# Kernel optimization log

Measured on AMD Instinct MI355X. Metric: run time of the kernel, lower is better.

Reference implementation:

```python
import jax, jax.numpy as jnp
import numpy as np

M1, M2, M3 = 12, 12, 8
WIDTH = 32


def _spectral_conv(v, wr, wi):
    # v: [B, C, X, Y, T]; wr/wi: [4, Ci, Co, M1, M2, M3]
    B, C, X, Y, T = v.shape
    vft = jnp.fft.rfftn(v, axes=(-3, -2, -1))  # [B,C,X,Y,T//2+1] complex
    w = wr.astype(jnp.complex64) + 1j * wi.astype(jnp.complex64)
    mul = lambda blk, ww: jnp.einsum('bixyz,ioxyz->boxyz', blk, ww)
    out = jnp.zeros((B, wr.shape[2], X, Y, T // 2 + 1), dtype=vft.dtype)
    out = out.at[:, :, :M1, :M2, :M3].set(mul(vft[:, :, :M1, :M2, :M3], w[0]))
    out = out.at[:, :, -M1:, :M2, :M3].set(mul(vft[:, :, -M1:, :M2, :M3], w[1]))
    out = out.at[:, :, :M1, -M2:, :M3].set(mul(vft[:, :, :M1, -M2:, :M3], w[2]))
    out = out.at[:, :, -M1:, -M2:, :M3].set(mul(vft[:, :, -M1:, -M2:, :M3], w[3]))
    return jnp.fft.irfftn(out, s=(X, Y, T), axes=(-3, -2, -1))


def _conv1x1(v, w, b):
    # v: [B,C,X,Y,T]; w: [Co,Ci]; b: [Co]
    return jnp.einsum('bixyz,oi->boxyz', v, w) + b[None, :, None, None, None]


def setup_inputs() -> dict:
    key = jax.random.key(0)
    ks = jax.random.split(key, 24)
    B, X, Y, T = 8, 64, 64, 40
    W = WIDTH
    scale = 1.0 / (W * W)
    d = {}
    d['h'] = jax.random.normal(ks[0], (B, X, Y, T, 2), dtype=jnp.float32)
    d['x'] = jax.random.normal(ks[1], (B, X, Y, T, 3), dtype=jnp.float32)
    d['fc0_w'] = jax.random.normal(ks[2], (5, W), dtype=jnp.float32) * 0.3
    d['fc0_b'] = jnp.zeros((W,), dtype=jnp.float32)
    for i, name in enumerate(['sc0', 'sc1', 'sc3']):
        d[name + '_wr'] = scale * jax.random.uniform(ks[3 + 2 * i], (4, W, W, M1, M2, M3), dtype=jnp.float32)
        d[name + '_wi'] = scale * jax.random.uniform(ks[4 + 2 * i], (4, W, W, M1, M2, M3), dtype=jnp.float32)
    for i, name in enumerate(['w0', 'w1', 'w3']):
        d[name + '_w'] = jax.random.normal(ks[9 + 2 * i], (W, W), dtype=jnp.float32) * (1.0 / np.sqrt(W))
        d[name + '_b'] = jnp.zeros((W,), dtype=jnp.float32)
    d['fc1_w'] = jax.random.normal(ks[15], (W, 64), dtype=jnp.float32) * (1.0 / np.sqrt(W))
    d['fc1_b'] = jnp.zeros((64,), dtype=jnp.float32)
    d['fc2_w'] = jax.random.normal(ks[16], (64, 2), dtype=jnp.float32) * 0.125
    d['fc2_b'] = jnp.zeros((2,), dtype=jnp.float32)
    return d


def reference(h, x, fc0_w, fc0_b, sc0_wr, sc0_wi, sc1_wr, sc1_wi, sc3_wr, sc3_wi,
              w0_w, w0_b, w1_w, w1_b, w3_w, w3_b, fc1_w, fc1_b, fc2_w, fc2_b):
    v = jnp.concatenate((h, x), axis=-1)                 # [B,X,Y,T,5]
    v = v @ fc0_w + fc0_b                                # lift to width
    v = jnp.transpose(v, (0, 4, 1, 2, 3))                # [B,W,X,Y,T]
    v = jax.nn.gelu(_spectral_conv(v, sc0_wr, sc0_wi) + _conv1x1(v, w0_w, w0_b), approximate=False)
    v = jax.nn.gelu(_spectral_conv(v, sc1_wr, sc1_wi) + _conv1x1(v, w1_w, w1_b), approximate=False)
    v = _spectral_conv(v, sc3_wr, sc3_wi) + _conv1x1(v, w3_w, w3_b)
    v = jnp.transpose(v, (0, 2, 3, 4, 1))                # [B,X,Y,T,W]
    v = jax.nn.gelu(v @ fc1_w + fc1_b, approximate=False)
    return v @ fc2_w + fc2_b                             # [B,X,Y,T,2]
```

## Files before the change

kernel.cpp:

```cpp
#include <hip/hip_runtime.h>
#include <math.h>

#define BATCH 8
#define WID   32
#define NX    64
#define NY    64
#define NT    40
#define M1C   12
#define KT    8
#define KXC   24
#define KYC   24
#define NXY   (NX*NY)
#define NXYT  (NXY*NT)
#define NP    (BATCH*NXYT)

#define TWO_PI 6.283185307179586f

static __device__ __forceinline__ float gelu_f(float v){
  return 0.5f*v*(1.0f + erff(v*0.7071067811865476f));
}

static __device__ __forceinline__ void barrier_lds(){
  asm volatile("s_waitcnt lgkmcnt(0)\n\ts_barrier" ::: "memory");
}


template<bool LIFT>
__global__ __launch_bounds__(512) void k_fwd_ty(const float* __restrict__ V, float2* __restrict__ F2,
                                                const float* __restrict__ hin, const float* __restrict__ xin,
                                                const float* __restrict__ lw, const float* __restrict__ lb){
  __shared__ __align__(16) unsigned char smem[56320];
  float2* twy   = (float2*)(smem+43008);
  float2* f2out = (float2*)smem;
  float*  wT2   = (float*)(smem+55296);
  int tid = threadIdx.x;
  int h = tid >> 8, t8 = tid & 255;
  int b = blockIdx.x >> 6, x = blockIdx.x & 63;
  int c = t8 & 31, k = t8 >> 5;
  if constexpr(LIFT){
    if(tid<192){
      int c4=tid/24, rem=tid-24*c4, i=rem>>2, e=rem&3;
      wT2[tid] = (i<5)? lw[i*32 + 4*c4 + e] : 2.0f*lb[4*c4+e];
    }
    __syncthreads();
  }
  for(int i=tid;i<KYC*NY;i+=512){
    int ky=i>>6, y=i&63;
    int f = ky<M1C ? ky : ky+40;
    float ang = -TWO_PI*(float)((f*y)%NY)/(float)NY;
    twy[i] = make_float2(cosf(ang), sinf(ang));
  }
  float2 twr[20];
  #pragma unroll
  for(int t=0;t<20;t++){
    float ang = -TWO_PI*(float)((k*t)%NT)/(float)NT;
    twr[t] = make_float2(cosf(ang), sinf(ang));
  }
  int toff = (k&1)*20;
  float2 acc[KYC];
  #pragma unroll
  for(int q=0;q<KYC;q++) acc[q]=make_float2(0.f,0.f);
  const float4* src = (const float4*)(V + (size_t)(b*NX+x)*(NY*NT*WID));
  const float* hb = hin + (size_t)(b*NX+x)*(NY*NT)*2;
  const float* xb = xin + (size_t)(b*NX+x)*(NY*NT)*3;
  float* myb0 = (float*)(smem + h*21504);
  float* myb1 = myb0 + 2688;

  int s0 = t8;
  int c40 = s0&7, t0s = (s0>>3)%20, yl0 = s0/160;
  bool has1 = (t8 < 64);
  int s1 = t8 + 256;
  int c41 = s1&7, t1s = (s1>>3)%20, yl1 = s1/160;

  float4 pa0, pb0, pa1, pb1;
  float2 hA0,hB0,hA1,hB1;
  float xA00,xA01,xA02,xB00,xB01,xB02;
  float xA10,xA11,xA12,xB10,xB11,xB12;

#define TY_LOAD(G) do{ \
    if constexpr(LIFT){ \
      { size_t pt = (size_t)((2*(G)+yl0)*40 + t0s); \
        hA0 = *(const float2*)(hb + pt*2); \
        hB0 = *(const float2*)(hb + (pt+20)*2); \
        xA00 = xb[pt*3]; xA01 = xb[pt*3+1]; xA02 = xb[pt*3+2]; \
        xB00 = xb[(pt+20)*3]; xB01 = xb[(pt+20)*3+1]; xB02 = xb[(pt+20)*3+2]; } \
      if(has1){ size_t pt = (size_t)((2*(G)+yl1)*40 + t1s); \
        hA1 = *(const float2*)(hb + pt*2); \
        hB1 = *(const float2*)(hb + (pt+20)*2); \
        xA10 = xb[pt*3]; xA11 = xb[pt*3+1]; xA12 = xb[pt*3+2]; \
        xB10 = xb[(pt+20)*3]; xB11 = xb[(pt+20)*3+1]; xB12 = xb[(pt+20)*3+2]; } \
    } else { \
      pa0 = src[(2*(G) + yl0)*320 + t0s*8 + c40]; \
      pb0 = src[(2*(G) + yl0)*320 + t0s*8 + c40 + 160]; \
      if(has1){ \
        pa1 = src[(2*(G) + yl1)*320 + t1s*8 + c41]; \
        pb1 = src[(2*(G) + yl1)*320 + t1s*8 + c41 + 160]; \
      } \
    } \
  }while(0)

#define TY_STAGE(BUF) do{ \
    if constexpr(LIFT){ \
      const float* wrp = wT2 + c40*24; \
      float4 w0v = *(const float4*)(wrp); \
      float4 w1v = *(const float4*)(wrp+4); \
      float4 w2v = *(const float4*)(wrp+8); \
      float4 w3v = *(const float4*)(wrp+12); \
      float4 w4v = *(const float4*)(wrp+16); \
      float4 wbv = *(const float4*)(wrp+20); \
      float su0=hA0.x+hB0.x, su1=hA0.y+hB0.y, su2=xA00+xB00, su3=xA01+xB01, su4=xA02+xB02; \
      float sd0=hA0.x-hB0.x, sd1=hA0.y-hB0.y, sd2=xA00-xB00, sd3=xA01-xB01, sd4=xA02-xB02; \
      float* bse = (BUF) + yl0*1344 + t0s; \
      _Pragma("unroll") \
      for(int e=0;e<4;e++){ \
        float w0=((float*)&w0v)[e], w1=((float*)&w1v)[e], w2=((float*)&w2v)[e]; \
        float w3=((float*)&w3v)[e], w4=((float*)&w4v)[e], wb=((float*)&wbv)[e]; \
        bse[(4*c40+e)*42]      = wb + su0*w0 + su1*w1 + su2*w2 + su3*w3 + su4*w4; \
        bse[(4*c40+e)*42 + 20] =      sd0*w0 + sd1*w1 + sd2*w2 + sd3*w3 + sd4*w4; \
      } \
      if(has1){ \
        float tu0=hA1.x+hB1.x, tu1=hA1.y+hB1.y, tu2=xA10+xB10, tu3=xA11+xB11, tu4=xA12+xB12; \
        float td0=hA1.x-hB1.x, td1=hA1.y-hB1.y, td2=xA10-xB10, td3=xA11-xB11, td4=xA12-xB12; \
        float* bs1 = (BUF) + yl1*1344 + t1s; \
        _Pragma("unroll") \
        for(int e=0;e<4;e++){ \
          float w0=((float*)&w0v)[e], w1=((float*)&w1v)[e], w2=((float*)&w2v)[e]; \
          float w3=((float*)&w3v)[e], w4=((float*)&w4v)[e], wb=((float*)&wbv)[e]; \
          bs1[(4*c41+e)*42]      = wb + tu0*w0 + tu1*w1 + tu2*w2 + tu3*w3 + tu4*w4; \
          bs1[(4*c41+e)*42 + 20] =      td0*w0 + td1*w1 + td2*w2 + td3*w3 + td4*w4; \
        } \
      } \
    } else { \
      float* bse = (BUF) + yl0*1344 + t0s; \
      _Pragma("unroll") \
      for(int e=0;e<4;e++){ \
        float av=((float*)&pa0)[e], bv=((float*)&pb0)[e]; \
        bse[(4*c40+e)*42]      = av+bv; \
        bse[(4*c40+e)*42 + 20] = av-bv; \
      } \
      if(has1){ \
        float* bs1 = (BUF) + yl1*1344 + t1s; \
        _Pragma("unroll") \
        for(int e=0;e<4;e++){ \
          float av=((float*)&pa1)[e], bv=((float*)&pb1)[e]; \
          bs1[(4*c41+e)*42]      = av+bv; \
          bs1[(4*c41+e)*42 + 20] = av-bv; \
        } \
      } \
    } \
  }while(0)

  TY_LOAD(h);
  TY_STAGE(myb0);
  TY_LOAD(h+2);
  __syncthreads();

  #pragma unroll 1
  for(int it=0; it<16; ++it){
    int g = 2*it + h;
    const float* vb = (it&1) ? myb1 : myb0;
    float*       vn = (it&1) ? myb0 : myb1;
    if(it+1<16){
      TY_STAGE(vn);
      if(it+2<16){
        TY_LOAD(g+4);
      }
    }
    {
      const float* vp0 = vb + c*42 + toff;
      const float* vp1 = vp0 + 1344;
      float sr0=0.f,si0=0.f,sr1=0.f,si1=0.f;
      #pragma unroll
      for(int i5=0; i5<5; i5++){
        float2 a0 = *(const float2*)(vp0 + i5*4);
        float2 b0 = *(const float2*)(vp0 + i5*4 + 2);
        float2 a1 = *(const float2*)(vp1 + i5*4);
        float2 b1 = *(const float2*)(vp1 + i5*4 + 2);
        float2 w0=twr[i5*4], w1=twr[i5*4+1], w2=twr[i5*4+2], w3=twr[i5*4+3];
        sr0 += a0.x*w0.x + a0.y*w1.x + b0.x*w2.x + b0.y*w3.x;
        si0 += a0.x*w0.y + a0.y*w1.y + b0.x*w2.y + b0.y*w3.y;
        sr1 += a1.x*w0.x + a1.y*w1.x + b1.x*w2.x + b1.y*w3.x;
        si1 += a1.x*w0.y + a1.y*w1.y + b1.x*w2.y + b1.y*w3.y;
      }
      int y = 2*g;
      #pragma unroll
      for(int q=0;q<KYC;q++){
        float4 wy = *(const float4*)&twy[q*NY + y];
        acc[q].x += sr0*wy.x - si0*wy.y + sr1*wy.z - si1*wy.w;
        acc[q].y += sr0*wy.y + si0*wy.x + sr1*wy.w + si1*wy.z;
      }
    }
    barrier_lds();
  }
  if(h==0){
    #pragma unroll
    for(int q=0;q<KYC;q++) f2out[c*193 + q*8 + k] = acc[q];
  }
  __syncthreads();
  if(h==1){
    #pragma unroll
    for(int q=0;q<KYC;q++){
      float2 v = f2out[c*193 + q*8 + k];
      f2out[c*193 + q*8 + k] = make_float2(v.x+acc[q].x, v.y+acc[q].y);
    }
  }
  __syncthreads();
  for(int i=tid;i<WID*KYC*KT;i+=512){
    int cc=i/192, e=i-cc*192;
    F2[((size_t)(b*WID+cc)*NX + x)*(KYC*KT) + e] = f2out[cc*193 + e];
  }
#undef TY_LOAD
#undef TY_STAGE
}

__global__ __launch_bounds__(256) void k_fwd_x(const float2* __restrict__ F2, float2* __restrict__ F3){
  __shared__ float2 tile[NX*KT];
  __shared__ float2 twi[KXC*65];
  int tid=threadIdx.x;
  int bc = blockIdx.x / KYC;
  int ky = blockIdx.x - bc*KYC;
  for(int i=tid;i<NX*KT;i+=256){
    int xx=i/KT, kt=i-xx*KT;
    tile[i] = F2[((size_t)bc*NX + xx)*(KYC*KT) + ky*KT + kt];
  }
  for(int i=tid;i<KXC*NX;i+=256){
    int kx=i/NX, xx=i-kx*NX;
    int f = kx<M1C ? kx : kx+40;
    float ang = -TWO_PI*(float)((f*xx)%NX)/(float)NX;
    twi[kx*65+xx] = make_float2(cosf(ang), sinf(ang));
  }
  __syncthreads();
  for(int item=tid; item<KXC*KT; item+=256){
    int kx=item/KT, kt=item-kx*KT;
    float sr=0.f, si=0.f;
    #pragma unroll 8
    for(int xx=0;xx<NX;xx++){
      float2 a = tile[xx*KT+kt];
      float2 w = twi[kx*65+xx];
      sr += a.x*w.x - a.y*w.y;
      si += a.x*w.y + a.y*w.x;
    }
    F3[(size_t)bc*(KXC*KYC*KT) + kx*(KYC*KT) + ky*KT + kt] = make_float2(sr,si);
  }
}

__global__ __launch_bounds__(256) void k_mix(const float2* __restrict__ F3, const float* __restrict__ wr,
                                             const float* __restrict__ wi, float2* __restrict__ F4){
  __shared__ float2 f3s[BATCH*WID*KT];
  int tid = threadIdx.x;
  int kx = blockIdx.x / KYC, ky = blockIdx.x - kx*KYC;
  int mode0 = blockIdx.x * KT;
  int xp = (kx>=M1C), yp = (ky>=M1C);
  int m1 = kx - M1C*xp, m2 = ky - M1C*yp;
  int blk = xp + 2*yp;
  for(int i=tid;i<1024;i+=256){
    int row=i>>2, q=i&3;
    ((float4*)f3s)[row*4+q] = ((const float4*)(F3 + (size_t)row*4608 + mode0))[q];
  }
  int o = tid>>3, kt = tid&7;
  size_t wbase = (size_t)blk*1179648 + (size_t)o*1152 + m1*96 + m2*8 + kt;
  float wre[WID], wim[WID];
  #pragma unroll
  for(int i=0;i<WID;i++){
    wre[i] = wr[wbase + (size_t)i*36864];
    wim[i] = wi[wbase + (size_t)i*36864];
  }
  __syncthreads();
  #pragma unroll
  for(int b=0;b<BATCH;b++){
    float ar=0.f, ai=0.f;
    #pragma unroll
    for(int i=0;i<WID;i++){
      float2 a = f3s[(b*WID+i)*KT + kt];
      ar += a.x*wre[i] - a.y*wim[i];
      ai += a.x*wim[i] + a.y*wre[i];
    }
    F4[(size_t)(b*WID+o)*4608 + mode0 + kt] = make_float2(ar,ai);
  }
}

__global__ __launch_bounds__(256) void k_inv_x(const float2* __restrict__ F4, float2* __restrict__ F2){
  __shared__ float2 tile[KXC*KT];
  __shared__ float2 twi[NX*25];
  int tid=threadIdx.x;
  int bc = blockIdx.x / KYC, ky = blockIdx.x - (blockIdx.x/KYC)*KYC;
  for(int i=tid;i<KXC*KT;i+=256){
    int kx=i/KT, kt=i-kx*KT;
    tile[i] = F4[(size_t)bc*4608 + kx*(KYC*KT) + ky*KT + kt];
  }
  for(int i=tid;i<NX*KXC;i+=256){
    int xx=i/KXC, kx=i-xx*KXC;
    int f = kx<M1C ? kx : kx+40;
    float ang = TWO_PI*(float)((f*xx)%NX)/(float)NX;
    twi[xx*25+kx] = make_float2(cosf(ang)*(1.0f/64.0f), sinf(ang)*(1.0f/64.0f));
  }
  __syncthreads();
  for(int item=tid; item<NX*KT; item+=256){
    int xx=item/KT, kt=item-xx*KT;
    float sr=0.f, si=0.f;
    #pragma unroll 8
    for(int kx=0;kx<KXC;kx++){
      float2 a = tile[kx*KT+kt];
      float2 w = twi[xx*25+kx];
      sr += a.x*w.x - a.y*w.y;
      si += a.x*w.y + a.y*w.x;
    }
    F2[((size_t)bc*NX + xx)*(KYC*KT) + ky*KT + kt] = make_float2(sr,si);
  }
}

template<bool GELU, bool LIFT>
__global__ __launch_bounds__(256) void k_conv(const float2* __restrict__ F2, const float* __restrict__ wcv,
                                              const float* __restrict__ bcv, float* __restrict__ V,
                                              const float* __restrict__ hin, const float* __restrict__ xin,
                                              const float* __restrict__ lw, const float* __restrict__ lb){
  __shared__ __align__(16) unsigned char smem[35840];
  float*  vtA  = (float*)smem;
  float*  vtB  = (float*)(smem+10240);
  float2* ftc0 = (float2*)(smem+20480);
  float2* ftc1 = (float2*)(smem+24576);
  float2* twy  = (float2*)(smem+28672);
  float*  wT2  = (float*)(smem+34816);
  float2* f2h  = (float2*)smem;

  int tid=threadIdx.x;
  int b  = blockIdx.x >> 7;
  int x  = (blockIdx.x >> 1) & 63;
  int y0 = (blockIdx.x & 1) * 32;
  int cid = tid & 31, ktid = tid >> 5;
  int oid = tid & 31, tg  = tid >> 5;

  if constexpr(LIFT){
    if(tid<192){
      int c4=tid/24, rem=tid-24*c4, i=rem>>2, e=rem&3;
      wT2[tid] = (i<5)? lw[i*32 + 4*c4 + e] : lb[4*c4+e];
    }
  }

  float2 fr[KYC];
  #pragma unroll
  for(int half=0; half<2; half++){
    for(int i=tid;i<1536;i+=256){
      int cc=i/96, q=i-cc*96;
      ((float4*)f2h)[i] = *((const float4*)(F2 + ((size_t)(b*WID + half*16 + cc)*NX + x)*(KYC*KT)) + q);
    }
    __syncthreads();
    if((cid>>4) == half){
      const float2* fp = f2h + (cid&15)*192 + ktid;
      #pragma unroll
      for(int ky=0;ky<KYC;ky++) fr[ky] = fp[ky*8];
    }
    __syncthreads();
  }
  {
    float ts = (ktid==0 ? 1.0f : 2.0f) * (1.0f/(float)NT);
    #pragma unroll
    for(int ky=0;ky<KYC;ky++){ fr[ky].x *= ts; fr[ky].y *= ts; }
  }
  float wreg[WID];
  #pragma unroll
  for(int cc=0;cc<WID;cc++) wreg[cc] = wcv[oid*WID + cc];
  float breg = bcv[oid];
  float2 twtg[KT];
  #pragma unroll
  for(int k=0;k<KT;k++){
    float ang = 0.78539816339744831f*(float)((k*tg)&7);
    twtg[k] = make_float2(cosf(ang), sinf(ang));
  }
  for(int i=tid;i<32*KYC;i+=256){
    int yy=i/KYC, ky=i-yy*KYC;
    int f = ky<M1C ? ky : ky+40;
    float ang = TWO_PI*(float)((f*(y0+yy))%NY)/(float)NY;
    twy[i] = make_float2(cosf(ang)*(1.0f/64.0f), sinf(ang)*(1.0f/64.0f));
  }
  float* plane = V + (size_t)((b*NX+x)*NY + y0)*(NT*WID);
  const float4* gp = (const float4*)plane;
  const float* hbc = hin + (size_t)((b*NX+x)*NY + y0)*NT*2;
  const float* xbc = xin + (size_t)((b*NX+x)*NY + y0)*NT*3;
  bool has3 = tid < 128;
  int t0c = tid>>3;
  int yy1c = (tid>=64);
  int t1c = yy1c ? ((tid-64)>>3) : ((tid+256)>>3);
  int t2c = (tid+192)>>3;
  int c4c = tid&7;

  float4 rA, rB, rC;
  float2 hC0, hC1, hC2;
  float xC00,xC01,xC02,xC10,xC11,xC12,xC20,xC21,xC22;

#define CV_LOAD(P) do{ \
    if constexpr(LIFT){ \
      { size_t pt = (size_t)((2*(P))*40 + t0c); \
        hC0 = *(const float2*)(hbc + pt*2); \
        xC00 = xbc[pt*3]; xC01 = xbc[pt*3+1]; xC02 = xbc[pt*3+2]; } \
      { size_t pt = (size_t)((2*(P)+yy1c)*40 + t1c); \
        hC1 = *(const float2*)(hbc + pt*2); \
        xC10 = xbc[pt*3]; xC11 = xbc[pt*3+1]; xC12 = xbc[pt*3+2]; } \
      if(has3){ size_t pt = (size_t)((2*(P)+1)*40 + t2c); \
        hC2 = *(const float2*)(hbc + pt*2); \
        xC20 = xbc[pt*3]; xC21 = xbc[pt*3+1]; xC22 = xbc[pt*3+2]; } \
    } else { \
      const float4* q = gp + (size_t)(P)*640; \
      rA = q[tid]; rB = q[256+tid]; \
      if(has3) rC = q[512+tid]; \
    } \
  }while(0)

#define CV_STAGE(BUF) do{ \
    if constexpr(LIFT){ \
      const float* wrp = wT2 + c4c*24; \
      float4 w0v = *(const float4*)(wrp); \
      float4 w1v = *(const float4*)(wrp+4); \
      float4 w2v = *(const float4*)(wrp+8); \
      float4 w3v = *(const float4*)(wrp+12); \
      float4 w4v = *(const float4*)(wrp+16); \
      float4 wbv = *(const float4*)(wrp+20); \
      float4 v0, v1, v2; \
      _Pragma("unroll") \
      for(int e=0;e<4;e++){ \
        float w0=((float*)&w0v)[e], w1=((float*)&w1v)[e], w2=((float*)&w2v)[e]; \
        float w3=((float*)&w3v)[e], w4=((float*)&w4v)[e], wb=((float*)&wbv)[e]; \
        ((float*)&v0)[e] = wb + hC0.x*w0 + hC0.y*w1 + xC00*w2 + xC01*w3 + xC02*w4; \
        ((float*)&v1)[e] = wb + hC1.x*w0 + hC1.y*w1 + xC10*w2 + xC11*w3 + xC12*w4; \
        if(has3) ((float*)&v2)[e] = wb + hC2.x*w0 + hC2.y*w1 + xC20*w2 + xC21*w3 + xC22*w4; \
      } \
      ((float4*)(BUF))[tid] = v0; \
      ((float4*)(BUF))[256+tid] = v1; \
      if(has3) ((float4*)(BUF))[512+tid] = v2; \
    } else { \
      ((float4*)(BUF))[tid] = rA; \
      ((float4*)(BUF))[256+tid] = rB; \
      if(has3) ((float4*)(BUF))[512+tid] = rC; \
    } \
  }while(0)

  CV_LOAD(0);
  CV_STAGE(vtA);
  CV_LOAD(1);
  __syncthreads();

  constexpr float CJ[KT][5] = {
    {1.f, 1.f,          1.f,          1.f,          1.f         },
    {1.f, 0.98768834f,  0.95105652f,  0.89100652f,  0.80901699f },
    {1.f, 0.95105652f,  0.80901699f,  0.58778525f,  0.30901699f },
    {1.f, 0.89100652f,  0.58778525f,  0.15643447f, -0.30901699f },
    {1.f, 0.80901699f,  0.30901699f, -0.30901699f, -0.80901699f },
    {1.f, 0.70710678f,  0.f,         -0.70710678f, -1.f         },
    {1.f, 0.58778525f, -0.30901699f, -0.95105652f, -0.80901699f },
    {1.f, 0.45399050f, -0.58778525f, -0.98768834f, -0.30901699f },
  };
  constexpr float SJ[KT][5] = {
    {0.f, 0.f,          0.f,          0.f,          0.f         },
    {0.f, 0.15643447f,  0.30901699f,  0.45399050f,  0.58778525f },
    {0.f, 0.30901699f,  0.58778525f,  0.80901699f,  0.95105652f },
    {0.f, 0.45399050f,  0.80901699f,  0.98768834f,  0.95105652f },
    {0.f, 0.58778525f,  0.95105652f,  0.95105652f,  0.58778525f },
    {0.f, 0.70710678f,  1.f,          0.70710678f,  0.f         },
    {0.f, 0.80901699f,  0.95105652f,  0.30901699f, -0.58778525f },
    {0.f, 0.89100652f,  0.80901699f, -0.15643447f, -0.95105652f },
  };

  #pragma unroll 1
  for(int it=0; it<16; ++it){
    float*  vcur = (it&1) ? vtB  : vtA;
    float*  vnxt = (it&1) ? vtA  : vtB;
    float2* fcur = (it&1) ? ftc1 : ftc0;
    int yl = it*2;
    {
      const float2* tw0 = twy + (size_t)yl*KYC;
      const float2* tw1 = tw0 + KYC;
      float sr0=0.f, si0=0.f, sr1=0.f, si1=0.f;
      #pragma unroll
      for(int ky=0;ky<KYC;ky+=2){
        float2 a  = fr[ky];
        float2 b2 = fr[ky+1];
        float4 w0 = *(const float4*)&tw0[ky];
        float4 w1 = *(const float4*)&tw1[ky];
        sr0 += a.x*w0.x - a.y*w0.y + b2.x*w0.z - b2.y*w0.w;
        si0 += a.x*w0.y + a.y*w0.x + b2.x*w0.w + b2.y*w0.z;
        sr1 += a.x*w1.x - a.y*w1.y + b2.x*w1.z - b2.y*w1.w;
        si1 += a.x*w1.y + a.y*w1.x + b2.x*w1.w + b2.y*w1.z;
      }
      fcur[      ktid*32 + cid] = make_float2(sr0,si0);
      fcur[256 + ktid*32 + cid] = make_float2(sr1,si1);
    }
    barrier_lds();
    if(it+1 < 16){
      CV_STAGE(vnxt);
    }
    if(it+2 < 16){
      CV_LOAD(it+2);
    }
    #pragma unroll
    for(int yy=0; yy<2; yy++){
      const float2* fsrc = fcur + yy*256;
      const float*  vb   = vcur + yy*1280;
      float* outp = plane + (size_t)(yl+yy)*(NT*WID);
      float acc[5];
      #pragma unroll
      for(int j=0;j<5;j++) acc[j] = breg;
      #pragma unroll
      for(int k=0;k<KT;k++){
        float2 f = fsrc[k*32 + oid];
        float gx = f.x*twtg[k].x - f.y*twtg[k].y;
        float gy = f.x*twtg[k].y + f.y*twtg[k].x;
        #pragma unroll
        for(int j=0;j<5;j++) acc[j] += gx*CJ[k][j] - gy*SJ[k][j];
      }
      #pragma unroll
      for(int j=0;j<5;j++){
        int t = tg*5 + j;
        float a = acc[j];
        const float* vrow = vb + t*32;
        #pragma unroll
        for(int c4=0;c4<WID;c4+=4){
          float4 vv = *(const float4*)(vrow + c4);
          a += vv.x*wreg[c4] + vv.y*wreg[c4+1] + vv.z*wreg[c4+2] + vv.w*wreg[c4+3];
        }
        outp[t*32 + oid] = GELU ? gelu_f(a) : a;
      }
    }
  }
#undef CV_LOAD
#undef CV_STAGE
}

__global__ __launch_bounds__(256) void k_mlp(const float* __restrict__ V, const float* __restrict__ w1,
                                             const float* __restrict__ b1, const float* __restrict__ w2,
                                             const float* __restrict__ b2, float* __restrict__ out){
  __shared__ float sw1t[64*WID];
  __shared__ float sb1[64], sw2[128], sb2[2];
  int tid=threadIdx.x;
  for(int i=tid;i<64*WID;i+=256){ int j=i>>5, c=i&31; sw1t[i]=w1[c*64+j]; }
  if(tid<64) sb1[tid]=b1[tid];
  if(tid<128) sw2[tid]=w2[tid];
  if(tid<2) sb2[tid]=b2[tid];
  __syncthreads();
  size_t p0 = (size_t)blockIdx.x*1024 + (size_t)tid*4;
  float vv[128];
  const float4* vp = (const float4*)(V + p0*WID);
  #pragma unroll
  for(int q=0;q<32;q++) *((float4*)(vv+4*q)) = vp[q];
  float oa[8];
  #pragma unroll
  for(int pt=0;pt<4;pt++){ oa[2*pt]=sb2[0]; oa[2*pt+1]=sb2[1]; }
  #pragma unroll 4
  for(int j=0;j<64;j++){
    float a0=sb1[j], a1=a0, a2=a0, a3=a0;
    const float* wrow = sw1t + j*WID;
    #pragma unroll
    for(int c4=0;c4<WID;c4+=4){
      float4 w = *(const float4*)(wrow + c4);
      a0 += vv[     c4]*w.x + vv[     c4+1]*w.y + vv[     c4+2]*w.z + vv[     c4+3]*w.w;
      a1 += vv[32 + c4]*w.x + vv[32 + c4+1]*w.y + vv[32 + c4+2]*w.z + vv[32 + c4+3]*w.w;
      a2 += vv[64 + c4]*w.x + vv[64 + c4+1]*w.y + vv[64 + c4+2]*w.z + vv[64 + c4+3]*w.w;
      a3 += vv[96 + c4]*w.x + vv[96 + c4+1]*w.y + vv[96 + c4+2]*w.z + vv[96 + c4+3]*w.w;
    }
    a0=gelu_f(a0); a1=gelu_f(a1); a2=gelu_f(a2); a3=gelu_f(a3);
    float u0=sw2[2*j], u1=sw2[2*j+1];
    oa[0]+=a0*u0; oa[1]+=a0*u1; oa[2]+=a1*u0; oa[3]+=a1*u1;
    oa[4]+=a2*u0; oa[5]+=a2*u1; oa[6]+=a3*u0; oa[7]+=a3*u1;
  }
  float4* op = (float4*)(out + p0*2);
  op[0]=make_float4(oa[0],oa[1],oa[2],oa[3]);
  op[1]=make_float4(oa[4],oa[5],oa[6],oa[7]);
}

extern "C" void kernel_launch(void* const* d_in, const int* in_sizes, int n_in,
                              void* d_out, int out_size, void* d_ws, size_t ws_size,
                              hipStream_t stream){
  const float* h     = (const float*)d_in[0];
  const float* x     = (const float*)d_in[1];
  const float* fc0_w = (const float*)d_in[2];
  const float* fc0_b = (const float*)d_in[3];
  const float* scwr[3] = {(const float*)d_in[4], (const float*)d_in[6], (const float*)d_in[8]};
  const float* scwi[3] = {(const float*)d_in[5], (const float*)d_in[7], (const float*)d_in[9]};
  const float* cw[3]   = {(const float*)d_in[10], (const float*)d_in[12], (const float*)d_in[14]};
  const float* cb[3]   = {(const float*)d_in[11], (const float*)d_in[13], (const float*)d_in[15]};
  const float* fc1_w = (const float*)d_in[16];
  const float* fc1_b = (const float*)d_in[17];
  const float* fc2_w = (const float*)d_in[18];
  const float* fc2_b = (const float*)d_in[19];

  const size_t VSZ = (size_t)BATCH*WID*NXYT;
  float*  V  = (float*)d_ws;
  float2* F2 = (float2*)(V + VSZ);
  float2* F4 = F2 + (size_t)BATCH*WID*NX*KYC*KT;
  float2* F3 = (float2*)d_out;

  for(int L=0; L<3; L++){
    if(L==0) k_fwd_ty<true ><<<BATCH*NX, 512, 0, stream>>>(V, F2, h, x, fc0_w, fc0_b);
    else     k_fwd_ty<false><<<BATCH*NX, 512, 0, stream>>>(V, F2, h, x, fc0_w, fc0_b);
    k_fwd_x<<<(BATCH*WID)*KYC, 256, 0, stream>>>(F2, F3);
    k_mix<<<KXC*KYC, 256, 0, stream>>>(F3, scwr[L], scwi[L], F4);
    k_inv_x<<<(BATCH*WID)*KYC, 256, 0, stream>>>(F4, F2);
    if(L==0)      k_conv<true ,true ><<<BATCH*NX*2, 256, 0, stream>>>(F2, cw[0], cb[0], V, h, x, fc0_w, fc0_b);
    else if(L==1) k_conv<true ,false><<<BATCH*NX*2, 256, 0, stream>>>(F2, cw[1], cb[1], V, h, x, fc0_w, fc0_b);
    else          k_conv<false,false><<<BATCH*NX*2, 256, 0, stream>>>(F2, cw[2], cb[2], V, h, x, fc0_w, fc0_b);
  }
  k_mlp<<<NP/1024, 256, 0, stream>>>(V, fc1_w, fc1_b, fc2_w, fc2_b, (float*)d_out);
}
```

Measured before the change: 1.373 ms.

## Add radix-2 butterfly over y in forward T/Y DFT, halve block size

The forward T/Y DFT kernel now folds y and y+32 with a butterfly before the y-DFT, because the retained modes' twiddles only depend on parity. That halves the number of y-steps and shrinks the y-twiddle table, and the block drops from 512 to 256 threads, which removes the cross-half reduction through shared memory. Each thread does four loads and more register work per stage, and the lift bias is rescaled to 4x to match. Fewer threads per block and higher register use may lower occupancy.

```diff
diff --git a/kernel.cpp b/kernel.cpp
--- a/kernel.cpp
+++ b/kernel.cpp
@@ -26,29 +26,28 @@
 
 
 template<bool LIFT>
-__global__ __launch_bounds__(512) void k_fwd_ty(const float* __restrict__ V, float2* __restrict__ F2,
+__global__ __launch_bounds__(256) void k_fwd_ty(const float* __restrict__ V, float2* __restrict__ F2,
                                                 const float* __restrict__ hin, const float* __restrict__ xin,
                                                 const float* __restrict__ lw, const float* __restrict__ lb){
-  __shared__ __align__(16) unsigned char smem[56320];
-  float2* twy   = (float2*)(smem+43008);
+  __shared__ __align__(16) unsigned char smem[49920];
+  float2* twy2  = (float2*)(smem+43008);
+  float*  wT2   = (float*)(smem+49152);
   float2* f2out = (float2*)smem;
-  float*  wT2   = (float*)(smem+55296);
   int tid = threadIdx.x;
-  int h = tid >> 8, t8 = tid & 255;
   int b = blockIdx.x >> 6, x = blockIdx.x & 63;
-  int c = t8 & 31, k = t8 >> 5;
+  int c = tid & 31, k = tid >> 5;
   if constexpr(LIFT){
     if(tid<192){
       int c4=tid/24, rem=tid-24*c4, i=rem>>2, e=rem&3;
-      wT2[tid] = (i<5)? lw[i*32 + 4*c4 + e] : 2.0f*lb[4*c4+e];
+      wT2[tid] = (i<5)? lw[i*32 + 4*c4 + e] : 4.0f*lb[4*c4+e];
     }
     __syncthreads();
   }
-  for(int i=tid;i<KYC*NY;i+=512){
-    int ky=i>>6, y=i&63;
-    int f = ky<M1C ? ky : ky+40;
+  for(int i=tid;i<KYC*32;i+=256){
+    int q=i>>5, y=i&31;
+    int f = q<M1C ? q : q+40;
     float ang = -TWO_PI*(float)((f*y)%NY)/(float)NY;
-    twy[i] = make_float2(cosf(ang), sinf(ang));
+    twy2[i] = make_float2(cosf(ang), sinf(ang));
   }
   float2 twr[20];
   #pragma unroll
@@ -63,153 +62,148 @@
   const float4* src = (const float4*)(V + (size_t)(b*NX+x)*(NY*NT*WID));
   const float* hb = hin + (size_t)(b*NX+x)*(NY*NT)*2;
   const float* xb = xin + (size_t)(b*NX+x)*(NY*NT)*3;
-  float* myb0 = (float*)(smem + h*21504);
-  float* myb1 = myb0 + 2688;
-
-  int s0 = t8;
+  float* bf0 = (float*)smem;
+  float* bf1 = bf0 + 5376;
+
+  int s0 = tid;
   int c40 = s0&7, t0s = (s0>>3)%20, yl0 = s0/160;
-  bool has1 = (t8 < 64);
-  int s1 = t8 + 256;
-  int c41 = s1&7, t1s = (s1>>3)%20, yl1 = s1/160;
-
-  float4 pa0, pb0, pa1, pb1;
-  float2 hA0,hB0,hA1,hB1;
-  float xA00,xA01,xA02,xB00,xB01,xB02;
-  float xA10,xA11,xA12,xB10,xB11,xB12;
+  bool has1 = (tid < 64);
+  int t1s = ((tid>>3)+12);
+
+  float4 pa0,pb0,pc0,pd0, pa1,pb1,pc1,pd1;
+  float2 h10,h20,h30,h40, h11,h21,h31,h41;
+  float x10[3],x20[3],x30[3],x40[3], x11[3],x21[3],x31[3],x41[3];
 
 #define TY_LOAD(G) do{ \
     if constexpr(LIFT){ \
-      { size_t pt = (size_t)((2*(G)+yl0)*40 + t0s); \
-        hA0 = *(const float2*)(hb + pt*2); \
-        hB0 = *(const float2*)(hb + (pt+20)*2); \
-        xA00 = xb[pt*3]; xA01 = xb[pt*3+1]; xA02 = xb[pt*3+2]; \
-        xB00 = xb[(pt+20)*3]; xB01 = xb[(pt+20)*3+1]; xB02 = xb[(pt+20)*3+2]; } \
-      if(has1){ size_t pt = (size_t)((2*(G)+yl1)*40 + t1s); \
-        hA1 = *(const float2*)(hb + pt*2); \
-        hB1 = *(const float2*)(hb + (pt+20)*2); \
-        xA10 = xb[pt*3]; xA11 = xb[pt*3+1]; xA12 = xb[pt*3+2]; \
-        xB10 = xb[(pt+20)*3]; xB11 = xb[(pt+20)*3+1]; xB12 = xb[(pt+20)*3+2]; } \
+      { int p = (2*(G)+yl0)*40 + t0s; \
+        h10 = *(const float2*)(hb + (size_t)p*2);        h20 = *(const float2*)(hb + (size_t)(p+20)*2); \
+        h30 = *(const float2*)(hb + (size_t)(p+1280)*2); h40 = *(const float2*)(hb + (size_t)(p+1300)*2); \
+        for(int ii=0;ii<3;ii++){ x10[ii]=xb[(size_t)p*3+ii]; x20[ii]=xb[(size_t)(p+20)*3+ii]; \
+                                 x30[ii]=xb[(size_t)(p+1280)*3+ii]; x40[ii]=xb[(size_t)(p+1300)*3+ii]; } } \
+      if(has1){ int p = (2*(G)+1)*40 + t1s; \
+        h11 = *(const float2*)(hb + (size_t)p*2);        h21 = *(const float2*)(hb + (size_t)(p+20)*2); \
+        h31 = *(const float2*)(hb + (size_t)(p+1280)*2); h41 = *(const float2*)(hb + (size_t)(p+1300)*2); \
+        for(int ii=0;ii<3;ii++){ x11[ii]=xb[(size_t)p*3+ii]; x21[ii]=xb[(size_t)(p+20)*3+ii]; \
+                                 x31[ii]=xb[(size_t)(p+1280)*3+ii]; x41[ii]=xb[(size_t)(p+1300)*3+ii]; } } \
     } else { \
-      pa0 = src[(2*(G) + yl0)*320 + t0s*8 + c40]; \
-      pb0 = src[(2*(G) + yl0)*320 + t0s*8 + c40 + 160]; \
-      if(has1){ \
-        pa1 = src[(2*(G) + yl1)*320 + t1s*8 + c41]; \
-        pb1 = src[(2*(G) + yl1)*320 + t1s*8 + c41 + 160]; \
-      } \
+      { const float4* q0 = src + (size_t)(2*(G)+yl0)*320 + t0s*8 + c40; \
+        pa0 = q0[0]; pb0 = q0[160]; pc0 = q0[10240]; pd0 = q0[10400]; } \
+      if(has1){ const float4* q1 = src + (size_t)(2*(G)+1)*320 + t1s*8 + c40; \
+        pa1 = q1[0]; pb1 = q1[160]; pc1 = q1[10240]; pd1 = q1[10400]; } \
     } \
   }while(0)
 
+#define TY_BFLY_STORE(BUF, YL, TS, C4, A1, A2, A3, A4) do{ \
+    _Pragma("unroll") \
+    for(int e=0;e<4;e++){ \
+      float a1=((float*)&A1)[e], a2=((float*)&A2)[e], a3=((float*)&A3)[e], a4=((float*)&A4)[e]; \
+      float u13=a1+a3, d13=a1-a3, u24=a2+a4, d24=a2-a4; \
+      float* bse = (BUF) + (YL)*2688 + (4*(C4)+e)*42 + (TS); \
+      bse[0]    = u13+u24;   \
+      bse[20]   = u13-u24;   \
+      bse[1344] = d13+d24;   \
+      bse[1364] = d13-d24;   \
+    } \
+  }while(0)
+
+#define TY_LIFT_STORE(BUF, YL, TS, C4, H1, H2, H3, H4, X1, X2, X3, X4) do{ \
+    float s00[5], s01[5], s10[5], s11[5]; \
+    { float a=H1.x,b2=H2.x,c2=H3.x,d2=H4.x; s00[0]=(a+b2)+(c2+d2); s01[0]=(a-b2)+(c2-d2); s10[0]=(a+b2)-(c2+d2); s11[0]=(a-b2)-(c2-d2); } \
+    { float a=H1.y,b2=H2.y,c2=H3.y,d2=H4.y; s00[1]=(a+b2)+(c2+d2); s01[1]=(a-b2)+(c2-d2); s10[1]=(a+b2)-(c2+d2); s11[1]=(a-b2)-(c2-d2); } \
+    _Pragma("unroll") \
+    for(int ii=0;ii<3;ii++){ float a=X1[ii],b2=X2[ii],c2=X3[ii],d2=X4[ii]; \
+      s00[2+ii]=(a+b2)+(c2+d2); s01[2+ii]=(a-b2)+(c2-d2); s10[2+ii]=(a+b2)-(c2+d2); s11[2+ii]=(a-b2)-(c2-d2); } \
+    const float* wrp = wT2 + (C4)*24; \
+    float4 w0v = *(const float4*)(wrp); \
+    float4 w1v = *(const float4*)(wrp+4); \
+    float4 w2v = *(const float4*)(wrp+8); \
+    float4 w3v = *(const float4*)(wrp+12); \
+    float4 w4v = *(const float4*)(wrp+16); \
+    float4 wbv = *(const float4*)(wrp+20); \
+    _Pragma("unroll") \
+    for(int e=0;e<4;e++){ \
+      float w0=((float*)&w0v)[e], w1=((float*)&w1v)[e], w2=((float*)&w2v)[e]; \
+      float w3=((float*)&w3v)[e], w4=((float*)&w4v)[e], wb=((float*)&wbv)[e]; \
+      float* bse = (BUF) + (YL)*2688 + (4*(C4)+e)*42 + (TS); \
+      bse[0]    = wb + s00[0]*w0 + s00[1]*w1 + s00[2]*w2 + s00[3]*w3 + s00[4]*w4; \
+      bse[20]   =      s01[0]*w0 + s01[1]*w1 + s01[2]*w2 + s01[3]*w3 + s01[4]*w4; \
+      bse[1344] =      s10[0]*w0 + s10[1]*w1 + s10[2]*w2 + s10[3]*w3 + s10[4]*w4; \
+      bse[1364] =      s11[0]*w0 + s11[1]*w1 + s11[2]*w2 + s11[3]*w3 + s11[4]*w4; \
+    } \
+  }while(0)
+
 #define TY_STAGE(BUF) do{ \
     if constexpr(LIFT){ \
-      const float* wrp = wT2 + c40*24; \
-      float4 w0v = *(const float4*)(wrp); \
-      float4 w1v = *(const float4*)(wrp+4); \
-      float4 w2v = *(const float4*)(wrp+8); \
-      float4 w3v = *(const float4*)(wrp+12); \
-      float4 w4v = *(const float4*)(wrp+16); \
-      float4 wbv = *(const float4*)(wrp+20); \
-      float su0=hA0.x+hB0.x, su1=hA0.y+hB0.y, su2=xA00+xB00, su3=xA01+xB01, su4=xA02+xB02; \
-      float sd0=hA0.x-hB0.x, sd1=hA0.y-hB0.y, sd2=xA00-xB00, sd3=xA01-xB01, sd4=xA02-xB02; \
-      float* bse = (BUF) + yl0*1344 + t0s; \
-      _Pragma("unroll") \
-      for(int e=0;e<4;e++){ \
-        float w0=((float*)&w0v)[e], w1=((float*)&w1v)[e], w2=((float*)&w2v)[e]; \
-        float w3=((float*)&w3v)[e], w4=((float*)&w4v)[e], wb=((float*)&wbv)[e]; \
-        bse[(4*c40+e)*42]      = wb + su0*w0 + su1*w1 + su2*w2 + su3*w3 + su4*w4; \
-        bse[(4*c40+e)*42 + 20] =      sd0*w0 + sd1*w1 + sd2*w2 + sd3*w3 + sd4*w4; \
-      } \
-      if(has1){ \
-        float tu0=hA1.x+hB1.x, tu1=hA1.y+hB1.y, tu2=xA10+xB10, tu3=xA11+xB11, tu4=xA12+xB12; \
-        float td0=hA1.x-hB1.x, td1=hA1.y-hB1.y, td2=xA10-xB10, td3=xA11-xB11, td4=xA12-xB12; \
-        float* bs1 = (BUF) + yl1*1344 + t1s; \
-        _Pragma("unroll") \
-        for(int e=0;e<4;e++){ \
-          float w0=((float*)&w0v)[e], w1=((float*)&w1v)[e], w2=((float*)&w2v)[e]; \
-          float w3=((float*)&w3v)[e], w4=((float*)&w4v)[e], wb=((float*)&wbv)[e]; \
-          bs1[(4*c41+e)*42]      = wb + tu0*w0 + tu1*w1 + tu2*w2 + tu3*w3 + tu4*w4; \
-          bs1[(4*c41+e)*42 + 20] =      td0*w0 + td1*w1 + td2*w2 + td3*w3 + td4*w4; \
-        } \
-      } \
+      TY_LIFT_STORE(BUF, yl0, t0s, c40, h10, h20, h30, h40, x10, x20, x30, x40); \
+      if(has1) TY_LIFT_STORE(BUF, 1, t1s, c40, h11, h21, h31, h41, x11, x21, x31, x41); \
     } else { \
-      float* bse = (BUF) + yl0*1344 + t0s; \
-      _Pragma("unroll") \
-      for(int e=0;e<4;e++){ \
-        float av=((float*)&pa0)[e], bv=((float*)&pb0)[e]; \
-        bse[(4*c40+e)*42]      = av+bv; \
-        bse[(4*c40+e)*42 + 20] = av-bv; \
-      } \
-      if(has1){ \
-        float* bs1 = (BUF) + yl1*1344 + t1s; \
-        _Pragma("unroll") \
-        for(int e=0;e<4;e++){ \
-          float av=((float*)&pa1)[e], bv=((float*)&pb1)[e]; \
-          bs1[(4*c41+e)*42]      = av+bv; \
-          bs1[(4*c41+e)*42 + 20] = av-bv; \
-        } \
-      } \
+      TY_BFLY_STORE(BUF, yl0, t0s, c40, pa0, pb0, pc0, pd0); \
+      if(has1) TY_BFLY_STORE(BUF, 1, t1s, c40, pa1, pb1, pc1, pd1); \
     } \
   }while(0)
 
-  TY_LOAD(h);
-  TY_STAGE(myb0);
-  TY_LOAD(h+2);
+  TY_LOAD(0);
+  TY_STAGE(bf0);
+  TY_LOAD(1);
   __syncthreads();
 
   #pragma unroll 1
-  for(int it=0; it<16; ++it){
-    int g = 2*it + h;
-    const float* vb = (it&1) ? myb1 : myb0;
-    float*       vn = (it&1) ? myb0 : myb1;
-    if(it+1<16){
+  for(int g=0; g<16; ++g){
+    const float* vb = (g&1) ? bf1 : bf0;
+    float*       vn = (g&1) ? bf0 : bf1;
+    if(g+1<16){
       TY_STAGE(vn);
-      if(it+2<16){
-        TY_LOAD(g+4);
+      if(g+2<16) TY_LOAD(g+2);
+    }
+    {
+      const float* p0 = vb + c*42 + toff;
+      float sru0=0.f,siu0=0.f,srd0=0.f,sid0=0.f;
+      float sru1=0.f,siu1=0.f,srd1=0.f,sid1=0.f;
+      #pragma unroll
+      for(int i5=0; i5<5; i5++){
+        float2 au0 = *(const float2*)(p0 + i5*4);
+        float2 bu0 = *(const float2*)(p0 + i5*4 + 2);
+        float2 ad0 = *(const float2*)(p0 + 1344 + i5*4);
+        float2 bd0 = *(const float2*)(p0 + 1344 + i5*4 + 2);
+        float2 au1 = *(const float2*)(p0 + 2688 + i5*4);
+        float2 bu1 = *(const float2*)(p0 + 2688 + i5*4 + 2);
+        float2 ad1 = *(const float2*)(p0 + 4032 + i5*4);
+        float2 bd1 = *(const float2*)(p0 + 4032 + i5*4 + 2);
+        float2 w0=twr[i5*4], w1=twr[i5*4+1], w2=twr[i5*4+2], w3=twr[i5*4+3];
+        sru0 += au0.x*w0.x + au0.y*w1.x + bu0.x*w2.x + bu0.y*w3.x;
+        siu0 += au0.x*w0.y + au0.y*w1.y + bu0.x*w2.y + bu0.y*w3.y;
+        srd0 += ad0.x*w0.x + ad0.y*w1.x + bd0.x*w2.x + bd0.y*w3.x;
+        sid0 += ad0.x*w0.y + ad0.y*w1.y + bd0.x*w2.y + bd0.y*w3.y;
+        sru1 += au1.x*w0.x + au1.y*w1.x + bu1.x*w2.x + bu1.y*w3.x;
+        siu1 += au1.x*w0.y + au1.y*w1.y + bu1.x*w2.y + bu1.y*w3.y;
+        srd1 += ad1.x*w0.x + ad1.y*w1.x + bd1.x*w2.x + bd1.y*w3.x;
+        sid1 += ad1.x*w0.y + ad1.y*w1.y + bd1.x*w2.y + bd1.y*w3.y;
       }
-    }
-    {
-      const float* vp0 = vb + c*42 + toff;
-      const float* vp1 = vp0 + 1344;
-      float sr0=0.f,si0=0.f,sr1=0.f,si1=0.f;
-      #pragma unroll
-      for(int i5=0; i5<5; i5++){
-        float2 a0 = *(const float2*)(vp0 + i5*4);
-        float2 b0 = *(const float2*)(vp0 + i5*4 + 2);
-        float2 a1 = *(const float2*)(vp1 + i5*4);
-        float2 b1 = *(const float2*)(vp1 + i5*4 + 2);
-        float2 w0=twr[i5*4], w1=twr[i5*4+1], w2=twr[i5*4+2], w3=twr[i5*4+3];
-        sr0 += a0.x*w0.x + a0.y*w1.x + b0.x*w2.x + b0.y*w3.x;
-        si0 += a0.x*w0.y + a0.y*w1.y + b0.x*w2.y + b0.y*w3.y;
-        sr1 += a1.x*w0.x + a1.y*w1.x + b1.x*w2.x + b1.y*w3.x;
-        si1 += a1.x*w0.y + a1.y*w1.y + b1.x*w2.y + b1.y*w3.y;
+      const float4* twp = (const float4*)&twy2[2*g];
+      #pragma unroll
+      for(int q=0;q<KYC;q++){
+        float4 w = twp[q*16];
+        float sr0 = (q&1)? srd0 : sru0;
+        float si0 = (q&1)? sid0 : siu0;
+        float sr1 = (q&1)? srd1 : sru1;
+        float si1 = (q&1)? sid1 : siu1;
+        acc[q].x += sr0*w.x - si0*w.y + sr1*w.z - si1*w.w;
+        acc[q].y += sr0*w.y + si0*w.x + sr1*w.w + si1*w.z;
       }
-      int y = 2*g;
-      #pragma unroll
-      for(int q=0;q<KYC;q++){
-        float4 wy = *(const float4*)&twy[q*NY + y];
-        acc[q].x += sr0*wy.x - si0*wy.y + sr1*wy.z - si1*wy.w;
-        acc[q].y += sr0*wy.y + si0*wy.x + sr1*wy.w + si1*wy.z;
-      }
     }
     barrier_lds();
   }
-  if(h==0){
-    #pragma unroll
-    for(int q=0;q<KYC;q++) f2out[c*193 + q*8 + k] = acc[q];
-  }
-  __syncthreads();
-  if(h==1){
-    #pragma unroll
-    for(int q=0;q<KYC;q++){
-      float2 v = f2out[c*193 + q*8 + k];
-      f2out[c*193 + q*8 + k] = make_float2(v.x+acc[q].x, v.y+acc[q].y);
-    }
-  }
-  __syncthreads();
-  for(int i=tid;i<WID*KYC*KT;i+=512){
+  #pragma unroll
+  for(int q=0;q<KYC;q++) f2out[c*193 + q*8 + k] = acc[q];
+  __syncthreads();
+  for(int i=tid;i<WID*KYC*KT;i+=256){
     int cc=i/192, e=i-cc*192;
     F2[((size_t)(b*WID+cc)*NX + x)*(KYC*KT) + e] = f2out[cc*193 + e];
   }
 #undef TY_LOAD
+#undef TY_BFLY_STORE
+#undef TY_LIFT_STORE
 #undef TY_STAGE
 }
 
@@ -589,8 +583,8 @@
   float2* F3 = (float2*)d_out;
 
   for(int L=0; L<3; L++){
-    if(L==0) k_fwd_ty<true ><<<BATCH*NX, 512, 0, stream>>>(V, F2, h, x, fc0_w, fc0_b);
-    else     k_fwd_ty<false><<<BATCH*NX, 512, 0, stream>>>(V, F2, h, x, fc0_w, fc0_b);
+    if(L==0) k_fwd_ty<true ><<<BATCH*NX, 256, 0, stream>>>(V, F2, h, x, fc0_w, fc0_b);
+    else     k_fwd_ty<false><<<BATCH*NX, 256, 0, stream>>>(V, F2, h, x, fc0_w, fc0_b);
     k_fwd_x<<<(BATCH*WID)*KYC, 256, 0, stream>>>(F2, F3);
     k_mix<<<KXC*KYC, 256, 0, stream>>>(F3, scwr[L], scwi[L], F4);
     k_inv_x<<<(BATCH*WID)*KYC, 256, 0, stream>>>(F4, F2);
```

Result: faster. 1.300 ms (-5.3%).
